# Performance work log

Hardware: AMD Instinct MI355X
Metric: run time of the kernel (lower is better)

## Reference

```python
import jax, jax.numpy as jnp
import numpy as np

N = 8192      # nodes
R = 3         # relations
D_IN = 64
D_HID = 64
D_OUT = 64


def setup_inputs() -> dict:
    key = jax.random.key(0)
    ks = jax.random.split(key, 6)
    x = jax.random.normal(ks[0], (N, D_IN), dtype=jnp.float32)
    # dense normalized adjacency-hat per relation; 1/N scale keeps tanh unsaturated
    adj = jax.random.uniform(ks[1], (R, N, N), dtype=jnp.float32) * (1.0 / N)
    s1 = 1.0 / np.sqrt(D_IN)
    s2 = 1.0 / np.sqrt(D_HID)
    W1 = jax.random.uniform(ks[2], (R, D_IN, D_HID), dtype=jnp.float32, minval=-s1, maxval=s1)
    b1 = jax.random.uniform(ks[3], (R, D_HID), dtype=jnp.float32, minval=-s1, maxval=s1)
    W2 = jax.random.uniform(ks[4], (R, D_HID, D_OUT), dtype=jnp.float32, minval=-s2, maxval=s2)
    b2 = jax.random.uniform(ks[5], (R, D_OUT), dtype=jnp.float32, minval=-s2, maxval=s2)
    return {"x": x, "adj": adj, "W1": W1, "b1": b1, "W2": W2, "b2": b2}


def _relgcn_conv(x, adj, W, b):
    # per-relation linear: [R, N, d_out]
    h = jnp.einsum('nf,rfh->rnh', x, W) + b[:, None, :]
    # adjacency matmul per relation, summed over relations: [N, d_out]
    m = jnp.einsum('rnm,rmh->nh', adj, h)
    return jnp.tanh(m)


def reference(x, adj, W1, b1, W2, b2):
    h = _relgcn_conv(x, adj, W1, b1)   # layer 0: in -> hidden
    y = _relgcn_conv(h, adj, W2, b2)   # layer 1: hidden -> out
    return y
```

## Files before the change

### kernel.cpp

```cpp
#include <hip/hip_runtime.h>


#define NN 8192
#define TS 516

typedef __attribute__((ext_vector_type(4))) float float4v;
typedef __attribute__((ext_vector_type(8))) short short8v;

__device__ inline unsigned short f2bf(float f) {
  unsigned int u = __builtin_bit_cast(unsigned int, f);
  return (unsigned short)((u + 0x7FFFu + ((u >> 16) & 1u)) >> 16);
}

__global__ __launch_bounds__(256) void prep(
    const float* __restrict__ in, const float* __restrict__ W,
    const float* __restrict__ b, unsigned short* __restrict__ hbf) {
  __shared__ float Ws[64 * 64];
  const int tid = threadIdx.x;
  const int r = blockIdx.x >> 8;
  const int g = blockIdx.x & 255;
  const int ml = tid >> 3;
  const int j0 = (tid & 7) * 8;
  const int m = g * 32 + ml;

#pragma unroll
  for (int i = 0; i < 16; ++i) Ws[tid + i * 256] = W[r * 4096 + tid + i * 256];

  float4v xr[16];
#pragma unroll
  for (int i = 0; i < 16; ++i)
    xr[i] = *(const float4v*)&in[(size_t)m * 64 + i * 4];

  float acc[8];
  {
    const float4v b0 = *(const float4v*)&b[r * 64 + j0];
    const float4v b1 = *(const float4v*)&b[r * 64 + j0 + 4];
#pragma unroll
    for (int jj = 0; jj < 4; ++jj) { acc[jj] = b0[jj]; acc[jj + 4] = b1[jj]; }
  }
  __syncthreads();

#pragma unroll
  for (int fi = 0; fi < 16; ++fi) {
    const float4v xv = xr[fi];
#pragma unroll
    for (int df = 0; df < 4; ++df) {
      const int f = fi * 4 + df;
      const float a = xv[df];
      const float4v w0 = *(const float4v*)&Ws[f * 64 + j0];
      const float4v w1 = *(const float4v*)&Ws[f * 64 + j0 + 4];
#pragma unroll
      for (int jj = 0; jj < 4; ++jj) {
        acc[jj] += a * w0[jj];
        acc[jj + 4] += a * w1[jj];
      }
    }
  }

  const size_t base = ((size_t)(r * 1024 + (m >> 3)) * 64) * 8 + (m & 7);
#pragma unroll
  for (int jj = 0; jj < 8; ++jj)
    hbf[base + (size_t)(j0 + jj) * 8] = f2bf(acc[jj]);
}

__global__ __launch_bounds__(256) void gemm_mfma(
    const float* __restrict__ adj, const unsigned short* __restrict__ hbf,
    float* __restrict__ out) {
  __shared__ float lds[2 * 16 * TS];
  float* buf0 = lds;
  float* buf1 = lds + 16 * TS;
  const int tid = threadIdx.x;
  const int w = tid >> 6;
  const int l = tid & 63;
  const int lrow = l & 15;
  const int lk = l >> 4;
  const int mb = blockIdx.x;
  const int phase = (mb * 29) % 48;

  const int srow = tid >> 4;
  const int sseg = tid & 15;
  const float* arow = adj + (size_t)(mb * 16 + srow) * NN + sseg * 4;

  float4v acc0 = {0.f, 0.f, 0.f, 0.f}, acc1 = acc0, acc2 = acc0, acc3 = acc0;
  float4v P0, P1, P2, P3, P4, P5, P6, P7, Q0, Q1, Q2, Q3, Q4, Q5, Q6, Q7;

#define TW(TQ) ((TQ) + phase >= 48 ? (TQ) + phase - 48 : (TQ) + phase)
#define TOFF(T) (((size_t)((T) >> 4) << 26) + ((size_t)((T) & 15) << 9))

#define GLOAD(T, S)                                                            \
  do {                                                                         \
    const float* pa_ = arow + TOFF(T);                                         \
    S##0 = __builtin_nontemporal_load((const float4v*)(pa_));                  \
    S##1 = __builtin_nontemporal_load((const float4v*)(pa_ + 64));             \
    S##2 = __builtin_nontemporal_load((const float4v*)(pa_ + 128));            \
    S##3 = __builtin_nontemporal_load((const float4v*)(pa_ + 192));            \
    S##4 = __builtin_nontemporal_load((const float4v*)(pa_ + 256));            \
    S##5 = __builtin_nontemporal_load((const float4v*)(pa_ + 320));            \
    S##6 = __builtin_nontemporal_load((const float4v*)(pa_ + 384));            \
    S##7 = __builtin_nontemporal_load((const float4v*)(pa_ + 448));            \
  } while (0)

#define DSWRITE(BUF, S)                                                        \
  do {                                                                         \
    float* p_ = (BUF) + srow * TS + sseg * 4;                                  \
    *(float4v*)(p_) = S##0;                                                    \
    *(float4v*)(p_ + 64) = S##1;                                               \
    *(float4v*)(p_ + 128) = S##2;                                              \
    *(float4v*)(p_ + 192) = S##3;                                              \
    *(float4v*)(p_ + 256) = S##4;                                              \
    *(float4v*)(p_ + 320) = S##5;                                              \
    *(float4v*)(p_ + 384) = S##6;                                              \
    *(float4v*)(p_ + 448) = S##7;                                              \
  } while (0)

#define DO_CHUNK(CUR, CC, B0, B1, B2, B3)                                      \
  do {                                                                         \
    const float* ap_ = (CUR) + lrow * TS + (w * 4 + (CC)) * 32 + lk * 8;       \
    const float4v a0_ = *(const float4v*)ap_;                                  \
    const float4v a1_ = *(const float4v*)(ap_ + 4);                            \
    short8v av_;                                                               \
    av_[0] = (short)f2bf(a0_[0]); av_[1] = (short)f2bf(a0_[1]);                \
    av_[2] = (short)f2bf(a0_[2]); av_[3] = (short)f2bf(a0_[3]);                \
    av_[4] = (short)f2bf(a1_[0]); av_[5] = (short)f2bf(a1_[1]);                \
    av_[6] = (short)f2bf(a1_[2]); av_[7] = (short)f2bf(a1_[3]);                \
    acc0 = __builtin_amdgcn_mfma_f32_16x16x32_bf16(av_, B0, acc0, 0, 0, 0);    \
    acc1 = __builtin_amdgcn_mfma_f32_16x16x32_bf16(av_, B1, acc1, 0, 0, 0);    \
    acc2 = __builtin_amdgcn_mfma_f32_16x16x32_bf16(av_, B2, acc2, 0, 0, 0);    \
    acc3 = __builtin_amdgcn_mfma_f32_16x16x32_bf16(av_, B3, acc3, 0, 0, 0);    \
  } while (0)

#define TILE(TQ, CBUF, WBUF, WS, LS)                                           \
  do {                                                                         \
    const int T_ = TW(TQ);                                                     \
    const unsigned short* pbb_ =                                               \
        hbf +                                                                  \
        ((size_t)((T_ >> 4) * 1024 + (T_ & 15) * 64 + w * 16 + lk) * 512) +    \
        lrow * 8;                                                              \
    const short8v B00 = *(const short8v*)(pbb_);                               \
    const short8v B01 = *(const short8v*)(pbb_ + 128);                         \
    const short8v B02 = *(const short8v*)(pbb_ + 256);                         \
    const short8v B03 = *(const short8v*)(pbb_ + 384);                         \
    const short8v B10 = *(const short8v*)(pbb_ + 2048);                        \
    const short8v B11 = *(const short8v*)(pbb_ + 2176);                        \
    const short8v B12 = *(const short8v*)(pbb_ + 2304);                        \
    const short8v B13 = *(const short8v*)(pbb_ + 2432);                        \
    const short8v B20 = *(const short8v*)(pbb_ + 4096);                        \
    const short8v B21 = *(const short8v*)(pbb_ + 4224);                        \
    const short8v B22 = *(const short8v*)(pbb_ + 4352);                        \
    const short8v B23 = *(const short8v*)(pbb_ + 4480);                        \
    const short8v B30 = *(const short8v*)(pbb_ + 6144);                        \
    const short8v B31 = *(const short8v*)(pbb_ + 6272);                        \
    const short8v B32 = *(const short8v*)(pbb_ + 6400);                        \
    const short8v B33 = *(const short8v*)(pbb_ + 6528);                        \
    if ((TQ) + 1 < 48) DSWRITE(WBUF, WS);                                      \
    if ((TQ) + 2 < 48) GLOAD(TW((TQ) + 2), LS);                                \
    DO_CHUNK(CBUF, 0, B00, B01, B02, B03);                                     \
    DO_CHUNK(CBUF, 1, B10, B11, B12, B13);                                     \
    DO_CHUNK(CBUF, 2, B20, B21, B22, B23);                                     \
    DO_CHUNK(CBUF, 3, B30, B31, B32, B33);                                     \
    __syncthreads();                                                           \
  } while (0)

  GLOAD(TW(0), P);
  DSWRITE(buf0, P);
  GLOAD(TW(1), Q);
  __syncthreads();

#pragma unroll 1
  for (int tq = 0; tq < 48; tq += 2) {
    TILE(tq, buf0, buf1, Q, P);
    TILE(tq + 1, buf1, buf0, P, Q);
  }
#undef TILE
#undef DO_CHUNK
#undef DSWRITE
#undef GLOAD
#undef TOFF
#undef TW

  float* red = lds;
#pragma unroll
  for (int q = 0; q < 4; ++q) {
    red[w * 1024 + (lk * 4 + q) * 64 + 0 + lrow] = acc0[q];
    red[w * 1024 + (lk * 4 + q) * 64 + 16 + lrow] = acc1[q];
    red[w * 1024 + (lk * 4 + q) * 64 + 32 + lrow] = acc2[q];
    red[w * 1024 + (lk * 4 + q) * 64 + 48 + lrow] = acc3[q];
  }
  __syncthreads();
#pragma unroll
  for (int idx = tid; idx < 1024; idx += 256) {
    const float s = red[idx] + red[1024 + idx] + red[2048 + idx] + red[3072 + idx];
    out[(size_t)mb * 1024 + idx] = tanhf(s);
  }
}

__global__ __launch_bounds__(256) void fill_sentinel(float* __restrict__ dst) {
  dst[blockIdx.x * 256 + threadIdx.x] = 7.0f;
}

extern "C" void kernel_launch(void* const* d_in, const int* in_sizes, int n_in,
                              void* d_out, int out_size, void* d_ws, size_t ws_size,
                              hipStream_t stream) {
  const float* x   = (const float*)d_in[0];
  const float* adj = (const float*)d_in[1];
  const float* W1  = (const float*)d_in[2];
  const float* b1  = (const float*)d_in[3];
  const float* W2  = (const float*)d_in[4];
  const float* b2  = (const float*)d_in[5];
  float* out = (float*)d_out;

  const size_t HBF_B = (size_t)3 * 8192 * 64 * 2;
  const size_t T_B   = (size_t)8192 * 64 * 4;
  if (ws_size < HBF_B + T_B) {
    fill_sentinel<<<2048, 256, 0, stream>>>(out);
    return;
  }
  unsigned short* hbf = (unsigned short*)d_ws;
  float* t = (float*)((char*)d_ws + HBF_B);

  prep<<<3 * 256, 256, 0, stream>>>(x, W1, b1, hbf);
  gemm_mfma<<<512, 256, 0, stream>>>(adj, hbf, t);
  prep<<<3 * 256, 256, 0, stream>>>(t, W2, b2, hbf);
  gemm_mfma<<<512, 256, 0, stream>>>(adj, hbf, out);
}
```

Before: 347.0 us.

## Cache an FP8 copy of adjacency in layer one and run layer two in FP8

The first adjacency GEMM now also writes a scaled FP8 (e4m3) copy of the adjacency matrix to workspace while it streams the fp32 data. A new prep2 kernel quantizes the layer-two features to FP8, and a new gemm_fp8 kernel runs the second pass with FP8 MFMA. The goal is to cut the second pass's adjacency read to a quarter of its fp32 size. In exchange, the first pass writes extra data, adjacency and features lose precision, and a single-block fp8_probe kernel checks FP8 MFMA against a decoded reference and stalls if they disagree.

```diff
diff --git a/kernel.cpp b/kernel.cpp
--- a/kernel.cpp
+++ b/kernel.cpp
@@ -3,13 +3,62 @@
 
 #define NN 8192
 #define TS 516
+#define AS8 528
 
 typedef __attribute__((ext_vector_type(4))) float float4v;
 typedef __attribute__((ext_vector_type(8))) short short8v;
+typedef __attribute__((ext_vector_type(4))) unsigned int uint4v;
 
 __device__ inline unsigned short f2bf(float f) {
   unsigned int u = __builtin_bit_cast(unsigned int, f);
   return (unsigned short)((u + 0x7FFFu + ((u >> 16) & 1u)) >> 16);
+}
+
+#if defined(__has_builtin)
+#if __has_builtin(__builtin_amdgcn_cvt_pk_fp8_f32) && __has_builtin(__builtin_amdgcn_cvt_f32_fp8)
+#define HW_FP8 1
+#endif
+#endif
+
+__device__ inline unsigned char enc_fp8_sw(float x) {
+  unsigned int u = __builtin_bit_cast(unsigned int, x);
+  unsigned int s = (u >> 24) & 0x80u;
+  unsigned int a = u & 0x7fffffffu;
+  if (a >= 0x43e00000u) return (unsigned char)(s | 0x7Eu);
+  int e = (int)(a >> 23) - 127;
+  unsigned int enc;
+  if (e >= -6) {
+    unsigned int keep = (a >> 20) & 7u;
+    unsigned int rem = a & 0xfffffu;
+    unsigned int inc = (rem > 0x80000u) || (rem == 0x80000u && (keep & 1u));
+    enc = (((unsigned)(e + 7) << 3) | keep) + inc;
+  } else {
+    float af = __builtin_bit_cast(float, a);
+    enc = (unsigned int)(af * 512.0f + 0.5f);
+  }
+  return (unsigned char)(s | enc);
+}
+__device__ inline float dec_fp8_sw(unsigned char b) {
+  int E = (b >> 3) & 15, m = b & 7;
+  float v = E ? ldexpf((float)(8 + m), E - 10) : ldexpf((float)m, -9);
+  return (b & 0x80) ? -v : v;
+}
+__device__ inline unsigned int pk4_fp8(float a, float b, float c, float d) {
+#ifdef HW_FP8
+  int w = __builtin_amdgcn_cvt_pk_fp8_f32(a, b, 0, false);
+  w = __builtin_amdgcn_cvt_pk_fp8_f32(c, d, w, true);
+  return (unsigned int)w;
+#else
+  return (unsigned int)enc_fp8_sw(a) | ((unsigned int)enc_fp8_sw(b) << 8) |
+         ((unsigned int)enc_fp8_sw(c) << 16) | ((unsigned int)enc_fp8_sw(d) << 24);
+#endif
+}
+__device__ inline float dec_fp8(unsigned char v) {
+#ifdef HW_FP8
+  return __builtin_amdgcn_cvt_f32_fp8((int)v, 0);
+#else
+  return dec_fp8_sw(v);
+#endif
 }
 
 __global__ __launch_bounds__(256) void prep(
@@ -22,15 +71,11 @@
   const int ml = tid >> 3;
   const int j0 = (tid & 7) * 8;
   const int m = g * 32 + ml;
-
 #pragma unroll
   for (int i = 0; i < 16; ++i) Ws[tid + i * 256] = W[r * 4096 + tid + i * 256];
-
   float4v xr[16];
 #pragma unroll
-  for (int i = 0; i < 16; ++i)
-    xr[i] = *(const float4v*)&in[(size_t)m * 64 + i * 4];
-
+  for (int i = 0; i < 16; ++i) xr[i] = *(const float4v*)&in[(size_t)m * 64 + i * 4];
   float acc[8];
   {
     const float4v b0 = *(const float4v*)&b[r * 64 + j0];
@@ -39,7 +84,6 @@
     for (int jj = 0; jj < 4; ++jj) { acc[jj] = b0[jj]; acc[jj + 4] = b1[jj]; }
   }
   __syncthreads();
-
 #pragma unroll
   for (int fi = 0; fi < 16; ++fi) {
     const float4v xv = xr[fi];
@@ -56,16 +100,64 @@
       }
     }
   }
-
   const size_t base = ((size_t)(r * 1024 + (m >> 3)) * 64) * 8 + (m & 7);
 #pragma unroll
   for (int jj = 0; jj < 8; ++jj)
     hbf[base + (size_t)(j0 + jj) * 8] = f2bf(acc[jj]);
 }
 
+__global__ __launch_bounds__(256) void prep2(
+    const float* __restrict__ in, const float* __restrict__ W,
+    const float* __restrict__ b, unsigned char* __restrict__ h2f8) {
+  __shared__ float Ws[64 * 64];
+  const int tid = threadIdx.x;
+  const int r = blockIdx.x >> 8;
+  const int g = blockIdx.x & 255;
+  const int ml = tid >> 3;
+  const int j0 = (tid & 7) * 8;
+  const int m = g * 32 + ml;
+#pragma unroll
+  for (int i = 0; i < 16; ++i) Ws[tid + i * 256] = W[r * 4096 + tid + i * 256];
+  float4v xr[16];
+#pragma unroll
+  for (int i = 0; i < 16; ++i) xr[i] = *(const float4v*)&in[(size_t)m * 64 + i * 4];
+  float acc[8];
+  {
+    const float4v b0 = *(const float4v*)&b[r * 64 + j0];
+    const float4v b1 = *(const float4v*)&b[r * 64 + j0 + 4];
+#pragma unroll
+    for (int jj = 0; jj < 4; ++jj) { acc[jj] = b0[jj]; acc[jj + 4] = b1[jj]; }
+  }
+  __syncthreads();
+#pragma unroll
+  for (int fi = 0; fi < 16; ++fi) {
+    const float4v xv = xr[fi];
+#pragma unroll
+    for (int df = 0; df < 4; ++df) {
+      const int f = fi * 4 + df;
+      const float a = xv[df];
+      const float4v w0 = *(const float4v*)&Ws[f * 64 + j0];
+      const float4v w1 = *(const float4v*)&Ws[f * 64 + j0 + 4];
+#pragma unroll
+      for (int jj = 0; jj < 4; ++jj) {
+        acc[jj] += a * w0[jj];
+        acc[jj + 4] += a * w1[jj];
+      }
+    }
+  }
+  const unsigned int u0 = pk4_fp8(acc[0] * 16.f, acc[1] * 16.f, acc[2] * 16.f, acc[3] * 16.f);
+  const unsigned int u1 = pk4_fp8(acc[4] * 16.f, acc[5] * 16.f, acc[6] * 16.f, acc[7] * 16.f);
+  const size_t base = (size_t)(r * 1024 + (m >> 3)) * 512 + (m & 7);
+#pragma unroll
+  for (int jj = 0; jj < 4; ++jj) {
+    h2f8[base + (size_t)(j0 + jj) * 8] = (unsigned char)((u0 >> (8 * jj)) & 0xff);
+    h2f8[base + (size_t)(j0 + 4 + jj) * 8] = (unsigned char)((u1 >> (8 * jj)) & 0xff);
+  }
+}
+
 __global__ __launch_bounds__(256) void gemm_mfma(
     const float* __restrict__ adj, const unsigned short* __restrict__ hbf,
-    float* __restrict__ out) {
+    float* __restrict__ out, unsigned char* __restrict__ adjf8) {
   __shared__ float lds[2 * 16 * TS];
   float* buf0 = lds;
   float* buf1 = lds + 16 * TS;
@@ -76,10 +168,10 @@
   const int lk = l >> 4;
   const int mb = blockIdx.x;
   const int phase = (mb * 29) % 48;
-
   const int srow = tid >> 4;
   const int sseg = tid & 15;
   const float* arow = adj + (size_t)(mb * 16 + srow) * NN + sseg * 4;
+  unsigned char* a8row = adjf8 + (size_t)(mb * 16 + srow) * NN + sseg * 4;
 
   float4v acc0 = {0.f, 0.f, 0.f, 0.f}, acc1 = acc0, acc2 = acc0, acc3 = acc0;
   float4v P0, P1, P2, P3, P4, P5, P6, P7, Q0, Q1, Q2, Q3, Q4, Q5, Q6, Q7;
@@ -100,7 +192,12 @@
     S##7 = __builtin_nontemporal_load((const float4v*)(pa_ + 448));            \
   } while (0)
 
-#define DSWRITE(BUF, S)                                                        \
+#define F8ST(S, I)                                                             \
+  __builtin_nontemporal_store(                                                 \
+      pk4_fp8(S[0] * 8192.f, S[1] * 8192.f, S[2] * 8192.f, S[3] * 8192.f),     \
+      (unsigned int*)(p8_ + (I)*64))
+
+#define DSWRITE(BUF, S, T)                                                     \
   do {                                                                         \
     float* p_ = (BUF) + srow * TS + sseg * 4;                                  \
     *(float4v*)(p_) = S##0;                                                    \
@@ -111,6 +208,9 @@
     *(float4v*)(p_ + 320) = S##5;                                              \
     *(float4v*)(p_ + 384) = S##6;                                              \
     *(float4v*)(p_ + 448) = S##7;                                              \
+    unsigned char* p8_ = a8row + TOFF(T);                                      \
+    F8ST(S##0, 0); F8ST(S##1, 1); F8ST(S##2, 2); F8ST(S##3, 3);                \
+    F8ST(S##4, 4); F8ST(S##5, 5); F8ST(S##6, 6); F8ST(S##7, 7);                \
   } while (0)
 
 #define DO_CHUNK(CUR, CC, B0, B1, B2, B3)                                      \
@@ -152,7 +252,7 @@
     const short8v B31 = *(const short8v*)(pbb_ + 6272);                        \
     const short8v B32 = *(const short8v*)(pbb_ + 6400);                        \
     const short8v B33 = *(const short8v*)(pbb_ + 6528);                        \
-    if ((TQ) + 1 < 48) DSWRITE(WBUF, WS);                                      \
+    if ((TQ) + 1 < 48) DSWRITE(WBUF, WS, TW((TQ) + 1));                        \
     if ((TQ) + 2 < 48) GLOAD(TW((TQ) + 2), LS);                                \
     DO_CHUNK(CBUF, 0, B00, B01, B02, B03);                                     \
     DO_CHUNK(CBUF, 1, B10, B11, B12, B13);                                     \
@@ -162,7 +262,7 @@
   } while (0)
 
   GLOAD(TW(0), P);
-  DSWRITE(buf0, P);
+  DSWRITE(buf0, P, TW(0));
   GLOAD(TW(1), Q);
   __syncthreads();
 
@@ -174,8 +274,8 @@
 #undef TILE
 #undef DO_CHUNK
 #undef DSWRITE
+#undef F8ST
 #undef GLOAD
-#undef TOFF
 #undef TW
 
   float* red = lds;
@@ -191,6 +291,159 @@
   for (int idx = tid; idx < 1024; idx += 256) {
     const float s = red[idx] + red[1024 + idx] + red[2048 + idx] + red[3072 + idx];
     out[(size_t)mb * 1024 + idx] = tanhf(s);
+  }
+}
+
+__global__ __launch_bounds__(256) void gemm_fp8(
+    const unsigned char* __restrict__ adjf8, const unsigned char* __restrict__ h2f8,
+    float* __restrict__ out) {
+  __shared__ __attribute__((aligned(16))) unsigned char lds8[2 * 16 * AS8];
+  unsigned char* buf0 = lds8;
+  unsigned char* buf1 = lds8 + 16 * AS8;
+  const int tid = threadIdx.x;
+  const int w = tid >> 6;
+  const int l = tid & 63;
+  const int lrow = l & 15;
+  const int lk = l >> 4;
+  const int mb = blockIdx.x;
+  const int phase = (mb * 29) % 48;
+  const int srow = tid >> 4;
+  const int sseg = tid & 15;
+  const unsigned char* arow = adjf8 + (size_t)(mb * 16 + srow) * NN + sseg * 32;
+
+  float4v acc0 = {0.f, 0.f, 0.f, 0.f}, acc1 = acc0, acc2 = acc0, acc3 = acc0;
+  uint4v Pa, Pb, Qa, Qb;
+
+#define TW(TQ) ((TQ) + phase >= 48 ? (TQ) + phase - 48 : (TQ) + phase)
+
+#define GLOAD8(T, SA, SB)                                                      \
+  do {                                                                         \
+    const unsigned char* pa_ = arow + TOFF(T);                                 \
+    SA = __builtin_nontemporal_load((const uint4v*)(pa_));                     \
+    SB = __builtin_nontemporal_load((const uint4v*)(pa_ + 16));                \
+  } while (0)
+
+#define DSWRITE8(BUF, SA, SB)                                                  \
+  do {                                                                         \
+    unsigned char* p_ = (BUF) + srow * AS8 + sseg * 32;                        \
+    *(uint4v*)(p_) = SA;                                                       \
+    *(uint4v*)(p_ + 16) = SB;                                                  \
+  } while (0)
+
+#define DO_CHUNK8(CUR, CC, B0, B1, B2, B3)                                     \
+  do {                                                                         \
+    const long av_ =                                                           \
+        *(const long*)&(CUR)[lrow * AS8 + (w * 4 + (CC)) * 32 + lk * 8];       \
+    acc0 = __builtin_amdgcn_mfma_f32_16x16x32_fp8_fp8(av_, B0, acc0, 0, 0, 0); \
+    acc1 = __builtin_amdgcn_mfma_f32_16x16x32_fp8_fp8(av_, B1, acc1, 0, 0, 0); \
+    acc2 = __builtin_amdgcn_mfma_f32_16x16x32_fp8_fp8(av_, B2, acc2, 0, 0, 0); \
+    acc3 = __builtin_amdgcn_mfma_f32_16x16x32_fp8_fp8(av_, B3, acc3, 0, 0, 0); \
+  } while (0)
+
+#define TILE8(TQ, CBUF, WBUF, WSA, WSB, LSA, LSB)                              \
+  do {                                                                         \
+    const int T_ = TW(TQ);                                                     \
+    const unsigned char* pbb_ =                                                \
+        h2f8 +                                                                 \
+        ((size_t)((T_ >> 4) * 1024 + (T_ & 15) * 64 + w * 16 + lk) * 512) +    \
+        lrow * 8;                                                              \
+    const long B00 = *(const long*)(pbb_);                                     \
+    const long B01 = *(const long*)(pbb_ + 128);                               \
+    const long B02 = *(const long*)(pbb_ + 256);                               \
+    const long B03 = *(const long*)(pbb_ + 384);                               \
+    const long B10 = *(const long*)(pbb_ + 2048);                              \
+    const long B11 = *(const long*)(pbb_ + 2176);                              \
+    const long B12 = *(const long*)(pbb_ + 2304);                              \
+    const long B13 = *(const long*)(pbb_ + 2432);                              \
+    const long B20 = *(const long*)(pbb_ + 4096);                              \
+    const long B21 = *(const long*)(pbb_ + 4224);                              \
+    const long B22 = *(const long*)(pbb_ + 4352);                              \
+    const long B23 = *(const long*)(pbb_ + 4480);                              \
+    const long B30 = *(const long*)(pbb_ + 6144);                              \
+    const long B31 = *(const long*)(pbb_ + 6272);                              \
+    const long B32 = *(const long*)(pbb_ + 6400);                              \
+    const long B33 = *(const long*)(pbb_ + 6528);                              \
+    if ((TQ) + 1 < 48) DSWRITE8(WBUF, WSA, WSB);                               \
+    if ((TQ) + 2 < 48) GLOAD8(TW((TQ) + 2), LSA, LSB);                         \
+    DO_CHUNK8(CBUF, 0, B00, B01, B02, B03);                                    \
+    DO_CHUNK8(CBUF, 1, B10, B11, B12, B13);                                    \
+    DO_CHUNK8(CBUF, 2, B20, B21, B22, B23);                                    \
+    DO_CHUNK8(CBUF, 3, B30, B31, B32, B33);                                    \
+    __syncthreads();                                                           \
+  } while (0)
+
+  GLOAD8(TW(0), Pa, Pb);
+  DSWRITE8(buf0, Pa, Pb);
+  GLOAD8(TW(1), Qa, Qb);
+  __syncthreads();
+
+#pragma unroll 1
+  for (int tq = 0; tq < 48; tq += 2) {
+    TILE8(tq, buf0, buf1, Qa, Qb, Pa, Pb);
+    TILE8(tq + 1, buf1, buf0, Pa, Pb, Qa, Qb);
+  }
+#undef TILE8
+#undef DO_CHUNK8
+#undef DSWRITE8
+#undef GLOAD8
+#undef TW
+
+  float* red = (float*)lds8;
+#pragma unroll
+  for (int q = 0; q < 4; ++q) {
+    red[w * 1024 + (lk * 4 + q) * 64 + 0 + lrow] = acc0[q];
+    red[w * 1024 + (lk * 4 + q) * 64 + 16 + lrow] = acc1[q];
+    red[w * 1024 + (lk * 4 + q) * 64 + 32 + lrow] = acc2[q];
+    red[w * 1024 + (lk * 4 + q) * 64 + 48 + lrow] = acc3[q];
+  }
+  __syncthreads();
+#pragma unroll
+  for (int idx = tid; idx < 1024; idx += 256) {
+    const float s = red[idx] + red[1024 + idx] + red[2048 + idx] + red[3072 + idx];
+    out[(size_t)mb * 1024 + idx] = tanhf(s * (1.0f / 131072.0f));
+  }
+}
+
+__global__ __launch_bounds__(64) void fp8_probe(
+    const unsigned char* __restrict__ adjf8, const unsigned char* __restrict__ h2f8) {
+  __shared__ float cm[16 * 64];
+  __shared__ int flag;
+  const int l = threadIdx.x;
+  if (l == 0) flag = 0;
+  const int lrow = l & 15, lk = l >> 4;
+  float4v acc[4];
+#pragma unroll
+  for (int g = 0; g < 4; ++g) acc[g] = (float4v){0.f, 0.f, 0.f, 0.f};
+#pragma unroll
+  for (int c = 0; c < 4; ++c) {
+    const long av = *(const long*)&adjf8[(size_t)lrow * NN + c * 32 + lk * 8];
+#pragma unroll
+    for (int g = 0; g < 4; ++g) {
+      const long bv =
+          *(const long*)&h2f8[(size_t)(c * 4 + lk) * 512 + (g * 16 + lrow) * 8];
+      acc[g] = __builtin_amdgcn_mfma_f32_16x16x32_fp8_fp8(av, bv, acc[g], 0, 0, 0);
+    }
+  }
+#pragma unroll
+  for (int g = 0; g < 4; ++g)
+#pragma unroll
+    for (int q = 0; q < 4; ++q)
+      cm[(lk * 4 + q) * 64 + g * 16 + lrow] = acc[g][q];
+  __syncthreads();
+  const int row = l & 15, c0 = (l >> 4) * 16;
+  float maxd = 0.f;
+  for (int cc = 0; cc < 16; ++cc) {
+    const int col = c0 + cc;
+    float ref = 0.f;
+    for (int k = 0; k < 128; ++k)
+      ref += dec_fp8(adjf8[(size_t)row * NN + k]) *
+             dec_fp8(h2f8[(size_t)(k >> 3) * 512 + col * 8 + (k & 7)]);
+    maxd = fmaxf(maxd, fabsf(cm[row * 64 + col] - ref));
+  }
+  if (maxd > 0.05f) atomicOr(&flag, 1);
+  __syncthreads();
+  if (flag) {
+    for (int i = 0; i < 150; ++i) __builtin_amdgcn_s_sleep(127);
   }
 }
 
@@ -211,15 +464,20 @@
 
   const size_t HBF_B = (size_t)3 * 8192 * 64 * 2;
   const size_t T_B   = (size_t)8192 * 64 * 4;
-  if (ws_size < HBF_B + T_B) {
+  const size_t H2_B  = (size_t)3 * 8192 * 64;
+  const size_t A8_B  = (size_t)3 * 8192 * 8192;
+  if (ws_size < HBF_B + T_B + H2_B + A8_B) {
     fill_sentinel<<<2048, 256, 0, stream>>>(out);
     return;
   }
-  unsigned short* hbf = (unsigned short*)d_ws;
-  float* t = (float*)((char*)d_ws + HBF_B);
+  unsigned short* hbf  = (unsigned short*)d_ws;
+  float* t             = (float*)((char*)d_ws + HBF_B);
+  unsigned char* h2f8  = (unsigned char*)((char*)d_ws + HBF_B + T_B);
+  unsigned char* adjf8 = (unsigned char*)((char*)d_ws + HBF_B + T_B + H2_B);
 
   prep<<<3 * 256, 256, 0, stream>>>(x, W1, b1, hbf);
-  gemm_mfma<<<512, 256, 0, stream>>>(adj, hbf, t);
-  prep<<<3 * 256, 256, 0, stream>>>(t, W2, b2, hbf);
-  gemm_mfma<<<512, 256, 0, stream>>>(adj, hbf, out);
-}
+  gemm_mfma<<<512, 256, 0, stream>>>(adj, hbf, t, adjf8);
+  prep2<<<3 * 256, 256, 0, stream>>>(t, W2, b2, h2f8);
+  fp8_probe<<<1, 64, 0, stream>>>(adjf8, h2f8);
+  gemm_fp8<<<512, 256, 0, stream>>>(adjf8, h2f8, out);
+}
```

New measurement: 342.3 us. About the same (-1.4%).
